# Kernel tuning notes

Hardware: AMD Instinct MI355X
Metric: run time of the kernel (lower is better)

The kernel has to match this reference:

```python
import jax, jax.numpy as jnp
import numpy as np

D_MODEL = 1024
N_HEADS = 16
HEAD_DIM = D_MODEL // N_HEADS


def setup_inputs() -> dict:
    key = jax.random.key(0)
    ks = jax.random.split(key, 9)
    B, S = 4, 2048
    x = jax.random.normal(ks[0], (B, S, D_MODEL), dtype=jnp.float32)
    init = 1.0 / np.sqrt(D_MODEL)
    def lin(kw, kb):
        W = jax.random.uniform(kw, (D_MODEL, D_MODEL), jnp.float32, -init, init)
        b = jax.random.uniform(kb, (D_MODEL,), jnp.float32, -init, init)
        return W, b
    Wq, bq = lin(ks[1], ks[2])
    Wk, bk = lin(ks[3], ks[4])
    Wv, bv = lin(ks[5], ks[6])
    Wo, bo = lin(ks[7], ks[8])
    return {"x": x, "Wq": Wq, "bq": bq, "Wk": Wk, "bk": bk,
            "Wv": Wv, "bv": bv, "Wo": Wo, "bo": bo}


def reference(x, Wq, bq, Wk, bk, Wv, bv, Wo, bo):
    B, S, _ = x.shape
    scale = jnp.sqrt(jnp.float32(HEAD_DIM))
    def split_heads(t):  # [B,S,D] -> [B,H,S,hd]
        return t.reshape(B, S, N_HEADS, HEAD_DIM).transpose(0, 2, 1, 3)
    q = split_heads(x @ Wq.T + bq)
    k = split_heads(x @ Wk.T + bk)
    v = split_heads(x @ Wv.T + bv)
    attn = jnp.einsum('bhqd,bhkd->bhqk', q, k) / scale
    attn = jax.nn.softmax(attn, axis=-1)
    out = jnp.einsum('bhqk,bhkd->bhqd', attn, v)  # [B,H,S,hd]
    out = out.transpose(0, 2, 1, 3).reshape(B, S, D_MODEL)
    return out @ Wo.T + bo
```

## Files before the change

### kernel.cpp

```cpp
#include <hip/hip_runtime.h>
#include <hip/hip_bf16.h>
#include <stdint.h>

typedef __attribute__((ext_vector_type(8))) short bf16x8;
typedef __attribute__((ext_vector_type(4))) float f32x4;
typedef __attribute__((ext_vector_type(16))) float f32x16;
typedef __attribute__((ext_vector_type(2))) unsigned int u32x2;
typedef unsigned short u16;

#define DEVI static __device__ __forceinline__

DEVI u16 f2bf(float f) {
  union { float f; uint32_t u; } x; x.f = f;
  uint32_t r = (x.u + 0x7FFFu + ((x.u >> 16) & 1u)) >> 16;
  return (u16)r;
}

DEVI void gload_lds16(const void* g, void* lds) {
  __builtin_amdgcn_global_load_lds(
      (const __attribute__((address_space(1))) void*)(void*)g,
      (__attribute__((address_space(3))) void*)lds, 16, 0, 0);
}

DEVI unsigned ldsaddr(const void* p) { return (unsigned)(uintptr_t)p; }

__global__ void cvt_all_kernel(const float* __restrict__ x,
                               const float* __restrict__ Wq, const float* __restrict__ Wk,
                               const float* __restrict__ Wv, const float* __restrict__ Wo,
                               const float* __restrict__ bq, const float* __restrict__ bk,
                               const float* __restrict__ bv,
                               u16* __restrict__ xb, u16* __restrict__ Wqkvb,
                               u16* __restrict__ Wob, float* __restrict__ bqkv) {
  const int X4 = 2097152;
  const int W4 = 262144;
  const int total = X4 + 4 * W4 + 768;
  int i = blockIdx.x * blockDim.x + threadIdx.x;
  const int stride = gridDim.x * blockDim.x;
  for (; i < total; i += stride) {
    if (i < X4) {
      float4 v = ((const float4*)x)[i];
      ((ushort4*)xb)[i] = make_ushort4(f2bf(v.x), f2bf(v.y), f2bf(v.z), f2bf(v.w));
    } else if (i < X4 + 4 * W4) {
      int j = i - X4;
      int which = j >> 18;
      int o = j & (W4 - 1);
      const float* src = which == 0 ? Wq : which == 1 ? Wk : which == 2 ? Wv : Wo;
      u16* dst = (which == 3) ? Wob : (Wqkvb + (size_t)which * 1048576);
      float4 v = ((const float4*)src)[o];
      ((ushort4*)dst)[o] = make_ushort4(f2bf(v.x), f2bf(v.y), f2bf(v.z), f2bf(v.w));
    } else {
      int j = i - X4 - 4 * W4;
      int which = j >> 8;
      int o = j & 255;
      const float* src = which == 0 ? bq : which == 1 ? bk : bv;
      ((float4*)bqkv)[which * 256 + o] = ((const float4*)src)[o];
    }
  }
}

template<int OUT_BF16>
__global__ __launch_bounds__(256, 2)
void gemm_bt_kernel(const u16* __restrict__ A, const u16* __restrict__ B,
                    const float* __restrict__ bias, void* __restrict__ C,
                    int M, int N, int K, int scale_cols, float scale_val) {
  __shared__ u16 As[128 * 32];
  __shared__ u16 Bs[128 * 32];
  const int tid = threadIdx.x;
  const int l = tid & 63;
  const int w = tid >> 6;
  const int bm = blockIdx.y, bn = blockIdx.x;
  const int wm = w >> 1, wn = w & 1;

  f32x4 acc[4][4] = {};

  const int srow = w * 32 + (l >> 2);
  const int scol = (l & 3) * 8;
  const u16* gA0 = A + (size_t)(bm * 128 + srow) * K + scol;
  const u16* gA1 = gA0 + (size_t)16 * K;
  const u16* gB0 = B + (size_t)(bn * 128 + srow) * K + scol;
  const u16* gB1 = gB0 + (size_t)16 * K;
  u16* lA0 = As + w * 1024;
  u16* lA1 = As + w * 1024 + 512;
  u16* lB0 = Bs + w * 1024;
  u16* lB1 = Bs + w * 1024 + 512;

  const int ar = wm * 64 + (l & 15);
  const int br = wn * 64 + (l & 15);
  const int kb = (l >> 4) * 8;

  for (int k0 = 0; k0 < K; k0 += 32) {
    __syncthreads();
    gload_lds16(gA0 + k0, lA0);
    gload_lds16(gA1 + k0, lA1);
    gload_lds16(gB0 + k0, lB0);
    gload_lds16(gB1 + k0, lB1);
    __syncthreads();
    bf16x8 af[4], bfr[4];
#pragma unroll
    for (int mf = 0; mf < 4; ++mf)
      af[mf] = *(const bf16x8*)&As[(ar + mf * 16) * 32 + kb];
#pragma unroll
    for (int nf = 0; nf < 4; ++nf)
      bfr[nf] = *(const bf16x8*)&Bs[(br + nf * 16) * 32 + kb];
#pragma unroll
    for (int mf = 0; mf < 4; ++mf)
#pragma unroll
      for (int nf = 0; nf < 4; ++nf)
        acc[mf][nf] = __builtin_amdgcn_mfma_f32_16x16x32_bf16(af[mf], bfr[nf], acc[mf][nf], 0, 0, 0);
  }

  const int rbase = bm * 128 + wm * 64 + (l >> 4) * 4;
  const int cbase = bn * 128 + wn * 64 + (l & 15);
#pragma unroll
  for (int nf = 0; nf < 4; ++nf) {
    int col = cbase + nf * 16;
    float bsv = bias[col];
    float sc = (col < scale_cols) ? scale_val : 1.0f;
#pragma unroll
    for (int mf = 0; mf < 4; ++mf) {
#pragma unroll
      for (int j = 0; j < 4; ++j) {
        int row = rbase + mf * 16 + j;
        float v = (acc[mf][nf][j] + bsv) * sc;
        if (OUT_BF16) ((u16*)C)[(size_t)row * N + col] = f2bf(v);
        else          ((float*)C)[(size_t)row * N + col] = v;
      }
    }
  }
}

__global__ __launch_bounds__(256, 3)
void attn_kernel(const u16* __restrict__ QKV, u16* __restrict__ O) {
  __shared__ u16 Ks[2][4096];
  __shared__ u16 Vs[2][4096];

  const int tid = threadIdx.x;
  const int l = tid & 63, w = tid >> 6;
  const int hi = l >> 5, c = l & 31;
  const int bh = blockIdx.y, b = bh >> 4, h = bh & 15;
  const int qb = blockIdx.x * 128 + w * 32;
  const size_t rowbase = (size_t)b * 2048;

  bf16x8 qf[4];
  {
    const u16* Qp = QKV + (rowbase + qb + c) * 3072 + h * 64 + hi * 8;
#pragma unroll
    for (int kk = 0; kk < 4; ++kk) qf[kk] = *(const bf16x8*)(Qp + kk * 16);
  }

  const int kd0 = (w * 2 + 0) * 64 + l;
  const int kd1 = (w * 2 + 1) * 64 + l;
  const int rK0 = kd0 >> 3, dbK0 = (kd0 & 7) ^ (rK0 & 7);
  const int rK1 = kd1 >> 3, dbK1 = (kd1 & 7) ^ (rK1 & 7);
  const u16* srcK0 = QKV + (rowbase + rK0) * 3072 + 1024 + h * 64 + dbK0 * 8;
  const u16* srcK1 = QKV + (rowbase + rK1) * 3072 + 1024 + h * 64 + dbK1 * 8;
  const int kV0 = (kd0 >> 5) * 4 + ((kd0 >> 1) & 3), dV0 = ((kd0 >> 3) & 3) * 16 + (kd0 & 1) * 8;
  const int kV1 = (kd1 >> 5) * 4 + ((kd1 >> 1) & 3), dV1 = ((kd1 >> 3) & 3) * 16 + (kd1 & 1) * 8;
  const u16* srcV0 = QKV + (rowbase + kV0) * 3072 + 2048 + h * 64 + dV0;
  const u16* srcV1 = QKV + (rowbase + kV1) * 3072 + 2048 + h * 64 + dV1;

#define STAGE(buf, tile) { \
    const size_t koff = (size_t)(tile) * 64 * 3072; \
    gload_lds16(srcK0 + koff, &Ks[buf][(w * 2 + 0) * 512]); \
    gload_lds16(srcK1 + koff, &Ks[buf][(w * 2 + 1) * 512]); \
    gload_lds16(srcV0 + koff, &Vs[buf][(w * 2 + 0) * 512]); \
    gload_lds16(srcV1 + koff, &Vs[buf][(w * 2 + 1) * 512]); \
  }

  int koffs[4];
#pragma unroll
  for (int kk = 0; kk < 4; ++kk) koffs[kk] = (((kk * 2 + hi) ^ (c & 7)) * 8);
  const int kbase = c * 64;

  const unsigned vbase = ldsaddr(&Vs[0][0]) + (unsigned)(hi * 1024 + (c >> 4) * 128 + (c & 15) * 8);

  const short ONEB = (short)0x3F80;
  const bf16x8 ones = {ONEB, ONEB, ONEB, ONEB, ONEB, ONEB, ONEB, ONEB};

  f32x16 o0 = {0,0,0,0,0,0,0,0,0,0,0,0,0,0,0,0};
  f32x16 o1 = {0,0,0,0,0,0,0,0,0,0,0,0,0,0,0,0};
  f32x16 osum = {0,0,0,0,0,0,0,0,0,0,0,0,0,0,0,0};

  STAGE(0, 0);
  __syncthreads();

  for (int t = 0; t < 32; ++t) {
    const int cur = t & 1;
    if (t < 31) STAGE(cur ^ 1, t + 1);

    const u16* kp = &Ks[cur][0];
    bf16x8 kf[2][4];
#pragma unroll
    for (int kb = 0; kb < 2; ++kb)
#pragma unroll
      for (int kk = 0; kk < 4; ++kk)
        kf[kb][kk] = *(const bf16x8*)&kp[kbase + kb * 2048 + koffs[kk]];

    f32x16 s0 = {0,0,0,0,0,0,0,0,0,0,0,0,0,0,0,0};
    f32x16 s1 = {0,0,0,0,0,0,0,0,0,0,0,0,0,0,0,0};
#pragma unroll
    for (int kk = 0; kk < 4; ++kk) {
      s0 = __builtin_amdgcn_mfma_f32_32x32x16_bf16(kf[0][kk], qf[kk], s0, 0, 0, 0);
      s1 = __builtin_amdgcn_mfma_f32_32x32x16_bf16(kf[1][kk], qf[kk], s1, 0, 0, 0);
    }

#pragma unroll
    for (int r = 0; r < 16; ++r) {
      s0[r] = __builtin_amdgcn_exp2f(s0[r]);
      s1[r] = __builtin_amdgcn_exp2f(s1[r]);
    }

    bf16x8 pa[4];
#define PP(r) ((r) < 16 ? s0[(r)] : s1[(r) - 16])
#pragma unroll
    for (int i = 0; i < 4; ++i) {
      unsigned a0, a1, b0, b1;
      asm("v_cvt_pk_bf16_f32 %0, %1, %2" : "=v"(a0) : "v"(PP(8*i+0)), "v"(PP(8*i+1)));
      asm("v_cvt_pk_bf16_f32 %0, %1, %2" : "=v"(a1) : "v"(PP(8*i+2)), "v"(PP(8*i+3)));
      asm("v_cvt_pk_bf16_f32 %0, %1, %2" : "=v"(b0) : "v"(PP(8*i+4)), "v"(PP(8*i+5)));
      asm("v_cvt_pk_bf16_f32 %0, %1, %2" : "=v"(b1) : "v"(PP(8*i+6)), "v"(PP(8*i+7)));
      unsigned t0 = hi ? a0 : b0;
      unsigned t1 = hi ? a1 : b1;
      unsigned x0 = (unsigned)__shfl_xor((int)t0, 32, 64);
      unsigned x1 = (unsigned)__shfl_xor((int)t1, 32, 64);
      union { unsigned u[4]; bf16x8 v; } U;
      U.u[0] = hi ? x0 : a0;
      U.u[1] = hi ? x1 : a1;
      U.u[2] = hi ? b0 : x0;
      U.u[3] = hi ? b1 : x1;
      pa[i] = U.v;
    }
#undef PP

    const unsigned va = vbase + (unsigned)(cur * 8192);
    u32x2 tt[4][4];
#pragma unroll
    for (int ks = 0; ks < 4; ++ks) {
      unsigned va_ks = va + (unsigned)(ks * 2048);
      asm volatile("ds_read_b64_tr_b16 %0, %1 offset:0"   : "=v"(tt[ks][0]) : "v"(va_ks));
      asm volatile("ds_read_b64_tr_b16 %0, %1 offset:512" : "=v"(tt[ks][1]) : "v"(va_ks));
      asm volatile("ds_read_b64_tr_b16 %0, %1 offset:256" : "=v"(tt[ks][2]) : "v"(va_ks));
      asm volatile("ds_read_b64_tr_b16 %0, %1 offset:768" : "=v"(tt[ks][3]) : "v"(va_ks));
    }
    asm volatile("s_waitcnt lgkmcnt(0)" ::: "memory");
    __builtin_amdgcn_sched_barrier(0);
#pragma unroll
    for (int ks = 0; ks < 4; ++ks) {
      union { u32x2 d2[2]; bf16x8 v; } V0, V1;
      V0.d2[0] = tt[ks][0]; V0.d2[1] = tt[ks][1];
      V1.d2[0] = tt[ks][2]; V1.d2[1] = tt[ks][3];
      o0 = __builtin_amdgcn_mfma_f32_32x32x16_bf16(pa[ks], V0.v, o0, 0, 0, 0);
      o1 = __builtin_amdgcn_mfma_f32_32x32x16_bf16(pa[ks], V1.v, o1, 0, 0, 0);
      osum = __builtin_amdgcn_mfma_f32_32x32x16_bf16(pa[ks], ones, osum, 0, 0, 0);
    }

    __syncthreads();
  }

  u16* Op = O + (rowbase + qb) * 1024 + h * 64 + c;
#pragma unroll
  for (int r = 0; r < 16; ++r) {
    int q = (r & 3) + 8 * (r >> 2) + 4 * hi;
    float inv = 1.0f / osum[r];
    Op[(size_t)q * 1024]      = f2bf(o0[r] * inv);
    Op[(size_t)q * 1024 + 32] = f2bf(o1[r] * inv);
  }
#undef STAGE
}

extern "C" void kernel_launch(void* const* d_in, const int* in_sizes, int n_in,
                              void* d_out, int out_size, void* d_ws, size_t ws_size,
                              hipStream_t stream) {
  const float* x  = (const float*)d_in[0];
  const float* Wq = (const float*)d_in[1];
  const float* bq = (const float*)d_in[2];
  const float* Wk = (const float*)d_in[3];
  const float* bk = (const float*)d_in[4];
  const float* Wv = (const float*)d_in[5];
  const float* bv = (const float*)d_in[6];
  const float* Wo = (const float*)d_in[7];
  const float* bo = (const float*)d_in[8];
  float* out = (float*)d_out;

  char* ws = (char*)d_ws;
  u16*   xb    = (u16*)(ws);
  u16*   Wqkvb = (u16*)(ws + 16777216);
  u16*   Wob   = (u16*)(ws + 23068672);
  float* bqkv  = (float*)(ws + 25165824);
  u16*   QKV   = (u16*)(ws + 25178112);
  u16*   Oa    = (u16*)(ws + 75509760);

  cvt_all_kernel<<<2048, 256, 0, stream>>>(x, Wq, Wk, Wv, Wo, bq, bk, bv,
                                           xb, Wqkvb, Wob, bqkv);

  gemm_bt_kernel<1><<<dim3(24, 64), 256, 0, stream>>>(xb, Wqkvb, bqkv, QKV,
                                                      8192, 3072, 1024, 1024,
                                                      0.125f * 1.4426950408889634f);
  attn_kernel<<<dim3(16, 64), 256, 0, stream>>>(QKV, Oa);
  gemm_bt_kernel<0><<<dim3(8, 64), 256, 0, stream>>>(Oa, Wob, bo, out,
                                                     8192, 1024, 1024, 0, 1.0f);
}
```

Before: 205.9 us.

## Double query rows per wave in attention and compute row sums without MFMA

Each attention wave now handles 64 query rows (two 32-row groups) instead of 32. This doubles the reuse of every K/V tile read from LDS and halves the grid. The softmax denominator is now built from per-lane partial exp sums combined with a cross-half shuffle, so the extra MFMA against a ones vector is gone. Softmax for the second query group is interleaved with the PV MFMAs of the first to hide latency. Register pressure rises, so the launch bound drops to 2 blocks per CU, which reduces occupancy.

```diff
diff --git a/kernel.cpp b/kernel.cpp
--- a/kernel.cpp
+++ b/kernel.cpp
@@ -129,7 +129,42 @@
   }
 }
 
-__global__ __launch_bounds__(256, 3)
+DEVI void softmax_pa(f32x16& sA, f32x16& sB, bf16x8* pa, float& lsum, int hi) {
+  float rs = 0.f;
+#pragma unroll
+  for (int r = 0; r < 16; ++r) { sA[r] = __builtin_amdgcn_exp2f(sA[r]); rs += sA[r]; }
+#pragma unroll
+  for (int r = 0; r < 16; ++r) { sB[r] = __builtin_amdgcn_exp2f(sB[r]); rs += sB[r]; }
+  lsum += rs + __shfl_xor(rs, 32, 64);
+#pragma unroll
+  for (int i = 0; i < 4; ++i) {
+    float p0 = (8 * i + 0 < 16) ? sA[(8 * i + 0) & 15] : sB[(8 * i + 0) & 15];
+    float p1 = (8 * i + 1 < 16) ? sA[(8 * i + 1) & 15] : sB[(8 * i + 1) & 15];
+    float p2 = (8 * i + 2 < 16) ? sA[(8 * i + 2) & 15] : sB[(8 * i + 2) & 15];
+    float p3 = (8 * i + 3 < 16) ? sA[(8 * i + 3) & 15] : sB[(8 * i + 3) & 15];
+    float p4 = (8 * i + 4 < 16) ? sA[(8 * i + 4) & 15] : sB[(8 * i + 4) & 15];
+    float p5 = (8 * i + 5 < 16) ? sA[(8 * i + 5) & 15] : sB[(8 * i + 5) & 15];
+    float p6 = (8 * i + 6 < 16) ? sA[(8 * i + 6) & 15] : sB[(8 * i + 6) & 15];
+    float p7 = (8 * i + 7 < 16) ? sA[(8 * i + 7) & 15] : sB[(8 * i + 7) & 15];
+    unsigned a0, a1, b0, b1;
+    asm("v_cvt_pk_bf16_f32 %0, %1, %2" : "=v"(a0) : "v"(p0), "v"(p1));
+    asm("v_cvt_pk_bf16_f32 %0, %1, %2" : "=v"(a1) : "v"(p2), "v"(p3));
+    asm("v_cvt_pk_bf16_f32 %0, %1, %2" : "=v"(b0) : "v"(p4), "v"(p5));
+    asm("v_cvt_pk_bf16_f32 %0, %1, %2" : "=v"(b1) : "v"(p6), "v"(p7));
+    unsigned t0 = hi ? a0 : b0;
+    unsigned t1 = hi ? a1 : b1;
+    unsigned x0 = (unsigned)__shfl_xor((int)t0, 32, 64);
+    unsigned x1 = (unsigned)__shfl_xor((int)t1, 32, 64);
+    union { unsigned u[4]; bf16x8 v; } U;
+    U.u[0] = hi ? x0 : a0;
+    U.u[1] = hi ? x1 : a1;
+    U.u[2] = hi ? b0 : x0;
+    U.u[3] = hi ? b1 : x1;
+    pa[i] = U.v;
+  }
+}
+
+__global__ __launch_bounds__(256, 2)
 void attn_kernel(const u16* __restrict__ QKV, u16* __restrict__ O) {
   __shared__ u16 Ks[2][4096];
   __shared__ u16 Vs[2][4096];
@@ -138,14 +173,18 @@
   const int l = tid & 63, w = tid >> 6;
   const int hi = l >> 5, c = l & 31;
   const int bh = blockIdx.y, b = bh >> 4, h = bh & 15;
-  const int qb = blockIdx.x * 128 + w * 32;
+  const int qb = blockIdx.x * 256 + w * 64;
   const size_t rowbase = (size_t)b * 2048;
 
-  bf16x8 qf[4];
+  bf16x8 qf0[4], qf1[4];
   {
-    const u16* Qp = QKV + (rowbase + qb + c) * 3072 + h * 64 + hi * 8;
-#pragma unroll
-    for (int kk = 0; kk < 4; ++kk) qf[kk] = *(const bf16x8*)(Qp + kk * 16);
+    const u16* Qp0 = QKV + (rowbase + qb + c) * 3072 + h * 64 + hi * 8;
+    const u16* Qp1 = QKV + (rowbase + qb + 32 + c) * 3072 + h * 64 + hi * 8;
+#pragma unroll
+    for (int kk = 0; kk < 4; ++kk) {
+      qf0[kk] = *(const bf16x8*)(Qp0 + kk * 16);
+      qf1[kk] = *(const bf16x8*)(Qp1 + kk * 16);
+    }
   }
 
   const int kd0 = (w * 2 + 0) * 64 + l;
@@ -174,12 +213,11 @@
 
   const unsigned vbase = ldsaddr(&Vs[0][0]) + (unsigned)(hi * 1024 + (c >> 4) * 128 + (c & 15) * 8);
 
-  const short ONEB = (short)0x3F80;
-  const bf16x8 ones = {ONEB, ONEB, ONEB, ONEB, ONEB, ONEB, ONEB, ONEB};
-
-  f32x16 o0 = {0,0,0,0,0,0,0,0,0,0,0,0,0,0,0,0};
-  f32x16 o1 = {0,0,0,0,0,0,0,0,0,0,0,0,0,0,0,0};
-  f32x16 osum = {0,0,0,0,0,0,0,0,0,0,0,0,0,0,0,0};
+  f32x16 o00 = {0,0,0,0,0,0,0,0,0,0,0,0,0,0,0,0};
+  f32x16 o01 = {0,0,0,0,0,0,0,0,0,0,0,0,0,0,0,0};
+  f32x16 o10 = {0,0,0,0,0,0,0,0,0,0,0,0,0,0,0,0};
+  f32x16 o11 = {0,0,0,0,0,0,0,0,0,0,0,0,0,0,0,0};
+  float lsum0 = 0.f, lsum1 = 0.f;
 
   STAGE(0, 0);
   __syncthreads();
@@ -196,41 +234,17 @@
       for (int kk = 0; kk < 4; ++kk)
         kf[kb][kk] = *(const bf16x8*)&kp[kbase + kb * 2048 + koffs[kk]];
 
-    f32x16 s0 = {0,0,0,0,0,0,0,0,0,0,0,0,0,0,0,0};
-    f32x16 s1 = {0,0,0,0,0,0,0,0,0,0,0,0,0,0,0,0};
+    f32x16 sA0 = {0,0,0,0,0,0,0,0,0,0,0,0,0,0,0,0};
+    f32x16 sB0 = {0,0,0,0,0,0,0,0,0,0,0,0,0,0,0,0};
+    f32x16 sA1 = {0,0,0,0,0,0,0,0,0,0,0,0,0,0,0,0};
+    f32x16 sB1 = {0,0,0,0,0,0,0,0,0,0,0,0,0,0,0,0};
 #pragma unroll
     for (int kk = 0; kk < 4; ++kk) {
-      s0 = __builtin_amdgcn_mfma_f32_32x32x16_bf16(kf[0][kk], qf[kk], s0, 0, 0, 0);
-      s1 = __builtin_amdgcn_mfma_f32_32x32x16_bf16(kf[1][kk], qf[kk], s1, 0, 0, 0);
-    }
-
-#pragma unroll
-    for (int r = 0; r < 16; ++r) {
-      s0[r] = __builtin_amdgcn_exp2f(s0[r]);
-      s1[r] = __builtin_amdgcn_exp2f(s1[r]);
-    }
-
-    bf16x8 pa[4];
-#define PP(r) ((r) < 16 ? s0[(r)] : s1[(r) - 16])
-#pragma unroll
-    for (int i = 0; i < 4; ++i) {
-      unsigned a0, a1, b0, b1;
-      asm("v_cvt_pk_bf16_f32 %0, %1, %2" : "=v"(a0) : "v"(PP(8*i+0)), "v"(PP(8*i+1)));
-      asm("v_cvt_pk_bf16_f32 %0, %1, %2" : "=v"(a1) : "v"(PP(8*i+2)), "v"(PP(8*i+3)));
-      asm("v_cvt_pk_bf16_f32 %0, %1, %2" : "=v"(b0) : "v"(PP(8*i+4)), "v"(PP(8*i+5)));
-      asm("v_cvt_pk_bf16_f32 %0, %1, %2" : "=v"(b1) : "v"(PP(8*i+6)), "v"(PP(8*i+7)));
-      unsigned t0 = hi ? a0 : b0;
-      unsigned t1 = hi ? a1 : b1;
-      unsigned x0 = (unsigned)__shfl_xor((int)t0, 32, 64);
-      unsigned x1 = (unsigned)__shfl_xor((int)t1, 32, 64);
-      union { unsigned u[4]; bf16x8 v; } U;
-      U.u[0] = hi ? x0 : a0;
-      U.u[1] = hi ? x1 : a1;
-      U.u[2] = hi ? b0 : x0;
-      U.u[3] = hi ? b1 : x1;
-      pa[i] = U.v;
-    }
-#undef PP
+      sA0 = __builtin_amdgcn_mfma_f32_32x32x16_bf16(kf[0][kk], qf0[kk], sA0, 0, 0, 0);
+      sB0 = __builtin_amdgcn_mfma_f32_32x32x16_bf16(kf[1][kk], qf0[kk], sB0, 0, 0, 0);
+      sA1 = __builtin_amdgcn_mfma_f32_32x32x16_bf16(kf[0][kk], qf1[kk], sA1, 0, 0, 0);
+      sB1 = __builtin_amdgcn_mfma_f32_32x32x16_bf16(kf[1][kk], qf1[kk], sB1, 0, 0, 0);
+    }
 
     const unsigned va = vbase + (unsigned)(cur * 8192);
     u32x2 tt[4][4];
@@ -242,28 +256,48 @@
       asm volatile("ds_read_b64_tr_b16 %0, %1 offset:256" : "=v"(tt[ks][2]) : "v"(va_ks));
       asm volatile("ds_read_b64_tr_b16 %0, %1 offset:768" : "=v"(tt[ks][3]) : "v"(va_ks));
     }
+
+    bf16x8 pa0[4];
+    softmax_pa(sA0, sB0, pa0, lsum0, hi);
+
     asm volatile("s_waitcnt lgkmcnt(0)" ::: "memory");
     __builtin_amdgcn_sched_barrier(0);
+
 #pragma unroll
     for (int ks = 0; ks < 4; ++ks) {
       union { u32x2 d2[2]; bf16x8 v; } V0, V1;
       V0.d2[0] = tt[ks][0]; V0.d2[1] = tt[ks][1];
       V1.d2[0] = tt[ks][2]; V1.d2[1] = tt[ks][3];
-      o0 = __builtin_amdgcn_mfma_f32_32x32x16_bf16(pa[ks], V0.v, o0, 0, 0, 0);
-      o1 = __builtin_amdgcn_mfma_f32_32x32x16_bf16(pa[ks], V1.v, o1, 0, 0, 0);
-      osum = __builtin_amdgcn_mfma_f32_32x32x16_bf16(pa[ks], ones, osum, 0, 0, 0);
+      o00 = __builtin_amdgcn_mfma_f32_32x32x16_bf16(pa0[ks], V0.v, o00, 0, 0, 0);
+      o01 = __builtin_amdgcn_mfma_f32_32x32x16_bf16(pa0[ks], V1.v, o01, 0, 0, 0);
+    }
+
+    bf16x8 pa1[4];
+    softmax_pa(sA1, sB1, pa1, lsum1, hi);
+
+#pragma unroll
+    for (int ks = 0; ks < 4; ++ks) {
+      union { u32x2 d2[2]; bf16x8 v; } V0, V1;
+      V0.d2[0] = tt[ks][0]; V0.d2[1] = tt[ks][1];
+      V1.d2[0] = tt[ks][2]; V1.d2[1] = tt[ks][3];
+      o10 = __builtin_amdgcn_mfma_f32_32x32x16_bf16(pa1[ks], V0.v, o10, 0, 0, 0);
+      o11 = __builtin_amdgcn_mfma_f32_32x32x16_bf16(pa1[ks], V1.v, o11, 0, 0, 0);
     }
 
     __syncthreads();
   }
 
-  u16* Op = O + (rowbase + qb) * 1024 + h * 64 + c;
+  u16* Op0 = O + (rowbase + qb) * 1024 + h * 64 + c;
+  u16* Op1 = O + (rowbase + qb + 32) * 1024 + h * 64 + c;
 #pragma unroll
   for (int r = 0; r < 16; ++r) {
     int q = (r & 3) + 8 * (r >> 2) + 4 * hi;
-    float inv = 1.0f / osum[r];
-    Op[(size_t)q * 1024]      = f2bf(o0[r] * inv);
-    Op[(size_t)q * 1024 + 32] = f2bf(o1[r] * inv);
+    float inv0 = 1.0f / __shfl(lsum0, q, 64);
+    float inv1 = 1.0f / __shfl(lsum1, q, 64);
+    Op0[(size_t)q * 1024]      = f2bf(o00[r] * inv0);
+    Op0[(size_t)q * 1024 + 32] = f2bf(o01[r] * inv0);
+    Op1[(size_t)q * 1024]      = f2bf(o10[r] * inv1);
+    Op1[(size_t)q * 1024 + 32] = f2bf(o11[r] * inv1);
   }
 #undef STAGE
 }
@@ -296,7 +330,7 @@
   gemm_bt_kernel<1><<<dim3(24, 64), 256, 0, stream>>>(xb, Wqkvb, bqkv, QKV,
                                                       8192, 3072, 1024, 1024,
                                                       0.125f * 1.4426950408889634f);
-  attn_kernel<<<dim3(16, 64), 256, 0, stream>>>(QKV, Oa);
+  attn_kernel<<<dim3(8, 64), 256, 0, stream>>>(QKV, Oa);
   gemm_bt_kernel<0><<<dim3(8, 64), 256, 0, stream>>>(Oa, Wob, bo, out,
                                                      8192, 1024, 1024, 0, 1.0f);
 }
```

Result: faster. 195.7 us (-5.0%).
